# Kernel optimization log

Hardware: AMD Instinct MI355X
Metric: run time of the kernel (lower is better)

## Reference

```python
import jax, jax.numpy as jnp
import numpy as np

E, HE, HD, V, B, S, T = 512, 1024, 1024, 32000, 64, 48, 48
PAD = 0


def lstm_cell(x, h, c, Wih, Whh, b):
    # torch gate order: i, f, g, o
    g = x @ Wih.T + h @ Whh.T + b
    i, f, gg, o = jnp.split(g, 4, axis=-1)
    c2 = jax.nn.sigmoid(f) * c + jax.nn.sigmoid(i) * jnp.tanh(gg)
    h2 = jax.nn.sigmoid(o) * jnp.tanh(c2)
    return h2, c2


def run_lstm(X, mask, Wih, Whh, b):
    # X: [S,B,E], mask: [S,B] bool; emulates packed-sequence semantics:
    # carry frozen and output zeroed at padded steps.
    hsz = Whh.shape[1]
    h0 = jnp.zeros((X.shape[1], hsz), X.dtype)

    def step(carry, xm):
        h, c = carry
        x, m = xm
        h2, c2 = lstm_cell(x, h, c, Wih, Whh, b)
        m = m[:, None]
        h = jnp.where(m, h2, h)
        c = jnp.where(m, c2, c)
        return (h, c), h * m

    (hT, cT), outs = jax.lax.scan(step, (h0, h0), (X, mask))
    return outs, hT, cT


def setup_inputs() -> dict:
    key = jax.random.key(0)
    ks = jax.random.split(key, 24)

    def rn(k, shape, scale=0.05):
        return jax.random.normal(k, shape, jnp.float32) * scale

    inp = {}
    inp['source_padded'] = jax.random.randint(ks[0], (S, B), 1, V).astype(jnp.int32)
    inp['target_padded'] = jax.random.randint(ks[1], (T, B), 1, V).astype(jnp.int32)
    lens = jnp.sort(jax.random.randint(ks[2], (B,), S // 2, S + 1))[::-1]
    inp['source_lengths'] = lens.at[0].set(S).astype(jnp.int32)
    # embeddings (padding row zeroed, matching nn.Embedding padding_idx)
    inp['src_emb'] = rn(ks[3], (V, E)).at[PAD].set(0.0)
    inp['tgt_emb'] = rn(ks[4], (V, E)).at[PAD].set(0.0)
    # bidirectional encoder LSTM (b = b_ih + b_hh combined)
    inp['enc_Wih_f'] = rn(ks[5], (4 * HE, E))
    inp['enc_Whh_f'] = rn(ks[6], (4 * HE, HE))
    inp['enc_b_f'] = rn(ks[7], (4 * HE,))
    inp['enc_Wih_b'] = rn(ks[8], (4 * HE, E))
    inp['enc_Whh_b'] = rn(ks[9], (4 * HE, HE))
    inp['enc_b_b'] = rn(ks[10], (4 * HE,))
    # decoder LSTMCell
    inp['dec_Wih'] = rn(ks[11], (4 * HD, E + HD))
    inp['dec_Whh'] = rn(ks[12], (4 * HD, HD))
    inp['dec_b'] = rn(ks[13], (4 * HD,))
    # projections (all bias=False in the original)
    inp['W_h'] = rn(ks[14], (HD, 2 * HE))
    inp['W_c'] = rn(ks[15], (HD, 2 * HE))
    inp['W_att'] = rn(ks[16], (HD, 2 * HE))
    inp['W_comb'] = rn(ks[17], (HE, 2 * HE + HD))
    inp['W_vocab'] = rn(ks[18], (V, HD))
    return inp


def reference(source_padded, target_padded, source_lengths, src_emb, tgt_emb,
              enc_Wih_f, enc_Whh_f, enc_b_f, enc_Wih_b, enc_Whh_b, enc_b_b,
              dec_Wih, dec_Whh, dec_b, W_h, W_c, W_att, W_comb, W_vocab):
    # ---- encode ----
    X = src_emb[source_padded]                       # [S,B,E]
    tpos = jnp.arange(S)[:, None]
    valid = tpos < source_lengths[None, :]           # [S,B]
    fwd_out, h_f, c_f = run_lstm(X, valid, enc_Wih_f, enc_Whh_f, enc_b_f)
    # reverse each sequence within its true length (packed-seq backward dir)
    rev_idx = jnp.where(valid, source_lengths[None, :] - 1 - tpos, tpos)
    Xrev = jnp.take_along_axis(X, rev_idx[:, :, None], axis=0)
    bwd_rev, h_b, c_b = run_lstm(Xrev, valid, enc_Wih_b, enc_Whh_b, enc_b_b)
    bwd_out = jnp.take_along_axis(bwd_rev, rev_idx[:, :, None], axis=0)
    enc_hiddens = jnp.concatenate([fwd_out, bwd_out], -1).transpose(1, 0, 2)  # [B,S,2HE]
    dec_h0 = jnp.concatenate([h_f, h_b], -1) @ W_h.T  # [B,HD]
    dec_c0 = jnp.concatenate([c_f, c_b], -1) @ W_c.T
    # ---- decode ----
    enc_proj = enc_hiddens @ W_att.T                 # [B,S,HD]
    pad_mask = ~valid.T                              # [B,S], True at padding
    Y = tgt_emb[target_padded[:-1]]                  # [T-1,B,E]

    def dstep(o_prev, y):
        ybar = jnp.concatenate([y, o_prev], -1)
        # NOTE: faithful to source bug - step() is always called with
        # dec_init_state, so the LSTMCell state resets every timestep.
        h_t, c_t = lstm_cell(ybar, dec_h0, dec_c0, dec_Wih, dec_Whh, dec_b)
        e = jnp.einsum('bsh,bh->bs', enc_proj, h_t)  # multiplicative attention
        e = jnp.where(pad_mask, -jnp.inf, e)
        alpha = jax.nn.softmax(e, -1)
        a = jnp.einsum('bs,bsd->bd', alpha, enc_hiddens)   # [B,2HE]
        O = jnp.tanh(jnp.concatenate([a, h_t], -1) @ W_comb.T)  # dropout=identity (eval)
        return O, O

    o0 = jnp.zeros((B, HD), X.dtype)
    _, combined = jax.lax.scan(dstep, o0, Y)          # [T-1,B,HE]
    # ---- loss-style scores ----
    P = jax.nn.log_softmax(combined @ W_vocab.T, -1)  # [T-1,B,V]
    gold = jnp.take_along_axis(P, target_padded[1:][:, :, None], axis=-1)[..., 0]
    tmask = (target_padded[1:] != PAD).astype(P.dtype)
    return (gold * tmask).sum(0)                      # [B]
```

## Files before the change

### kernel.cpp

```cpp
#include <hip/hip_runtime.h>
#include <math.h>


#define S_    48
#define B_    64
#define E_    512
#define H_    1024
#define H4_   4096
#define V_    32000
#define T1_   47
#define NROW_ 3008
#define NROWP 3072
#define NTV_  500
#define NBE   128
#define NBD   128

typedef __bf16 bf16x8 __attribute__((ext_vector_type(8)));
typedef float  f32x4  __attribute__((ext_vector_type(4)));
typedef unsigned short ushort_t;
typedef unsigned long long ull_t;

__device__ __forceinline__ float sigm(float x){ return 1.f/(1.f+expf(-x)); }
__device__ __forceinline__ unsigned short f2bs(float f){
  unsigned u=__float_as_uint(f); u+=0x7fffu+((u>>16)&1u); return (unsigned short)(u>>16);
}
__device__ __forceinline__ float b2f(ushort_t u){ return __uint_as_float(((unsigned)u)<<16); }
__device__ __forceinline__ void gload16(const ushort_t* g, ushort_t* l){
  __builtin_amdgcn_global_load_lds((const __attribute__((address_space(1))) void*)g,
                                   (__attribute__((address_space(3))) void*)l,16,0,0);
}

__device__ __forceinline__ void ast32(void* p, unsigned v){
  __hip_atomic_store((unsigned*)p,v,__ATOMIC_RELAXED,__HIP_MEMORY_SCOPE_AGENT);
}
__device__ __forceinline__ void ast64(void* p, ull_t v){
  __hip_atomic_store((ull_t*)p,v,__ATOMIC_RELAXED,__HIP_MEMORY_SCOPE_AGENT);
}

__device__ __forceinline__ void arrive(unsigned* flags, int idx, unsigned ep){
  if(threadIdx.x==0) ast32(&flags[idx*16], ep);
}
__device__ __forceinline__ void wait_flags(unsigned* flags, int n, unsigned ep){
  for(int i=threadIdx.x;i<n;i+=256){
    while(__hip_atomic_load(&flags[i*16],__ATOMIC_RELAXED,__HIP_MEMORY_SCOPE_AGENT)<ep){}
  }
  __syncthreads();
}

__device__ __forceinline__ void stage128(const ushort_t* src, int ld, int k0,
                                         ushort_t* lds, int w, int lane){
  const int rA=lane>>3, gA=lane&7;
#pragma unroll
  for(int i=0;i<4;i++){
    int rb=w*32+i*8;
    int row=rb+rA;
    gload16(src+(size_t)row*ld+k0+(((gA)^(row&7))*8), &lds[rb*64]);
  }
}

#define ACC_DECL \
  f32x4 c00={0,0,0,0},c01={0,0,0,0},c02={0,0,0,0},c03={0,0,0,0}, \
        c10={0,0,0,0},c11={0,0,0,0},c12={0,0,0,0},c13={0,0,0,0}, \
        c20={0,0,0,0},c21={0,0,0,0},c22={0,0,0,0},c23={0,0,0,0}, \
        c30={0,0,0,0},c31={0,0,0,0},c32={0,0,0,0},c33={0,0,0,0};

#define MFMA_ __builtin_amdgcn_mfma_f32_16x16x32_bf16
#define MMA_K64(AsB,BsB) do{ \
  _Pragma("unroll") \
  for(int ks_=0;ks_<2;ks_++){ \
    const int sw_=((ks_*4+l4)^l7)*8; \
    bf16x8 a0_=*(const bf16x8*)&(AsB)[(wm*64+ 0+l15)*64+sw_]; \
    bf16x8 a1_=*(const bf16x8*)&(AsB)[(wm*64+16+l15)*64+sw_]; \
    bf16x8 a2_=*(const bf16x8*)&(AsB)[(wm*64+32+l15)*64+sw_]; \
    bf16x8 a3_=*(const bf16x8*)&(AsB)[(wm*64+48+l15)*64+sw_]; \
    bf16x8 b0_=*(const bf16x8*)&(BsB)[(wn*64+ 0+l15)*64+sw_]; \
    bf16x8 b1_=*(const bf16x8*)&(BsB)[(wn*64+16+l15)*64+sw_]; \
    bf16x8 b2_=*(const bf16x8*)&(BsB)[(wn*64+32+l15)*64+sw_]; \
    bf16x8 b3_=*(const bf16x8*)&(BsB)[(wn*64+48+l15)*64+sw_]; \
    c00=MFMA_(a0_,b0_,c00,0,0,0); c01=MFMA_(a0_,b1_,c01,0,0,0); \
    c02=MFMA_(a0_,b2_,c02,0,0,0); c03=MFMA_(a0_,b3_,c03,0,0,0); \
    c10=MFMA_(a1_,b0_,c10,0,0,0); c11=MFMA_(a1_,b1_,c11,0,0,0); \
    c12=MFMA_(a1_,b2_,c12,0,0,0); c13=MFMA_(a1_,b3_,c13,0,0,0); \
    c20=MFMA_(a2_,b0_,c20,0,0,0); c21=MFMA_(a2_,b1_,c21,0,0,0); \
    c22=MFMA_(a2_,b2_,c22,0,0,0); c23=MFMA_(a2_,b3_,c23,0,0,0); \
    c30=MFMA_(a3_,b0_,c30,0,0,0); c31=MFMA_(a3_,b1_,c31,0,0,0); \
    c32=MFMA_(a3_,b2_,c32,0,0,0); c33=MFMA_(a3_,b3_,c33,0,0,0); \
  } \
}while(0)

__global__ __launch_bounds__(256)
void proj3(const ushort_t* __restrict__ Xb, const ushort_t* __restrict__ WfB, const float* __restrict__ bf,
           const ushort_t* __restrict__ XrB, const ushort_t* __restrict__ WbB, const float* __restrict__ bb,
           const ushort_t* __restrict__ Yb, const ushort_t* __restrict__ WyB,
           float* __restrict__ XpF, float* __restrict__ XpB, float* __restrict__ Yp)
{
  __shared__ __align__(16) ushort_t As[128*64];
  __shared__ __align__(16) ushort_t Bs[128*64];
  const ushort_t* A; const ushort_t* B; const float* bias; float* C;
  if(blockIdx.z==0){A=Xb;B=WfB;bias=bf;C=XpF;}
  else if(blockIdx.z==1){A=XrB;B=WbB;bias=bb;C=XpB;}
  else {A=Yb;B=WyB;bias=nullptr;C=Yp;}
  const int tid=threadIdx.x, w=tid>>6, lane=tid&63;
  const int wm=w>>1, wn=w&1;
  const int l15=lane&15, l4=lane>>4, l7=lane&7;
  const int m0=blockIdx.x*128, n0=blockIdx.y*128;
  ACC_DECL
  for(int k0=0;k0<E_;k0+=64){
    stage128(A+(size_t)m0*E_, E_, k0, As, w, lane);
    stage128(B+(size_t)n0*E_, E_, k0, Bs, w, lane);
    __syncthreads();
    MMA_K64(As,Bs);
    __syncthreads();
  }
  const int cr=l4*4, cc=l15;
#define PSTORE(CM,mi,ni) { int col=n0+wn*64+(ni)*16+cc; float bv=bias?bias[col]:0.f; \
  _Pragma("unroll") for(int j=0;j<4;j++){ int row=m0+wm*64+(mi)*16+cr+j; \
    C[(size_t)row*H4_+col]=CM[j]+bv; } }
  PSTORE(c00,0,0) PSTORE(c01,0,1) PSTORE(c02,0,2) PSTORE(c03,0,3)
  PSTORE(c10,1,0) PSTORE(c11,1,1) PSTORE(c12,1,2) PSTORE(c13,1,3)
  PSTORE(c20,2,0) PSTORE(c21,2,1) PSTORE(c22,2,2) PSTORE(c23,2,3)
  PSTORE(c30,3,0) PSTORE(c31,3,1) PSTORE(c32,3,2) PSTORE(c33,3,3)
#undef PSTORE
}

__global__ __launch_bounds__(256)
void bproj(const ushort_t* __restrict__ A, int lda,
           const ushort_t* __restrict__ B, int ldb, int K,
           ushort_t* __restrict__ Cb)
{
  __shared__ __align__(16) ushort_t As[128*64];
  __shared__ __align__(16) ushort_t Bs[128*64];
  const int tid=threadIdx.x, w=tid>>6, lane=tid&63;
  const int wm=w>>1, wn=w&1;
  const int l15=lane&15, l4=lane>>4, l7=lane&7;
  const int m0=blockIdx.x*128, n0=blockIdx.y*128;
  ACC_DECL
  for(int k0=0;k0<K;k0+=64){
    stage128(A+(size_t)m0*lda, lda, k0, As, w, lane);
    stage128(B+(size_t)n0*ldb, ldb, k0, Bs, w, lane);
    __syncthreads();
    MMA_K64(As,Bs);
    __syncthreads();
  }
  const int cr=l4*4, cc=l15;
#define BSTORE(CM,mi,ni) { int col=n0+wn*64+(ni)*16+cc; \
  _Pragma("unroll") for(int j=0;j<4;j++){ int row=m0+wm*64+(mi)*16+cr+j; \
    Cb[(size_t)row*H_+col]=f2bs(CM[j]); } }
  BSTORE(c00,0,0) BSTORE(c01,0,1) BSTORE(c02,0,2) BSTORE(c03,0,3)
  BSTORE(c10,1,0) BSTORE(c11,1,1) BSTORE(c12,1,2) BSTORE(c13,1,3)
  BSTORE(c20,2,0) BSTORE(c21,2,1) BSTORE(c22,2,2) BSTORE(c23,2,3)
  BSTORE(c30,3,0) BSTORE(c31,3,1) BSTORE(c32,3,2) BSTORE(c33,3,3)
#undef BSTORE
}

__global__ __launch_bounds__(256)
void mfma_vocab(const ushort_t* __restrict__ A, const ushort_t* __restrict__ B,
                const int* __restrict__ tgt,
                float* __restrict__ pmax, float* __restrict__ psum, float* __restrict__ gold)
{
  __shared__ __align__(16) ushort_t As[128*64];
  __shared__ __align__(16) ushort_t Bs[128*64];
  const int tid=threadIdx.x, w=tid>>6, lane=tid&63;
  const int wm=w>>1, wn=w&1;
  const int l15=lane&15, l4=lane>>4, l7=lane&7;
  const int m0=blockIdx.x*128, n0=blockIdx.y*128;
  ACC_DECL
  for(int k0=0;k0<H_;k0+=64){
    stage128(A+(size_t)m0*H_, H_, k0, As, w, lane);
    stage128(B+(size_t)n0*H_, H_, k0, Bs, w, lane);
    __syncthreads();
    MMA_K64(As,Bs);
    __syncthreads();
  }
  const int tile=blockIdx.y*2+wn;
  const int cc=l15;
#define VEPI(mi,R0,R1,R2,R3) { \
  _Pragma("unroll") for(int j=0;j<4;j++){ \
    int row=m0+wm*64+(mi)*16+l4*4+j; \
    float m=fmaxf(fmaxf(R0[j],R1[j]),fmaxf(R2[j],R3[j])); \
    for(int o=1;o<16;o<<=1) m=fmaxf(m,__shfl_xor(m,o,64)); \
    float s=expf(R0[j]-m)+expf(R1[j]-m)+expf(R2[j]-m)+expf(R3[j]-m); \
    for(int o=1;o<16;o<<=1) s+=__shfl_xor(s,o,64); \
    if(row<NROW_){ \
      if(cc==0){ pmax[(size_t)tile*NROWP+row]=m; psum[(size_t)tile*NROWP+row]=s; } \
      int g=tgt[((row>>6)+1)*B_+(row&63)]; \
      int lj=g-(n0+wn*64); \
      if(lj>=0&&lj<64&&(lj&15)==cc){ int q=lj>>4; \
        gold[row]= (q==0)?R0[j]:(q==1)?R1[j]:(q==2)?R2[j]:R3[j]; } \
    } } }
  VEPI(0,c00,c01,c02,c03)
  VEPI(1,c10,c11,c12,c13)
  VEPI(2,c20,c21,c22,c23)
  VEPI(3,c30,c31,c32,c33)
#undef VEPI
}

__global__ __launch_bounds__(256)
void enc_persist(const ushort_t* __restrict__ WhhB2,
                 const float* __restrict__ XpF, const float* __restrict__ XpB,
                 const int* __restrict__ lens,
                 ushort_t* __restrict__ hroll,
                 float* __restrict__ cst,
                 ushort_t* __restrict__ outF, ushort_t* __restrict__ outBR,
                 unsigned* __restrict__ flagsE)
{
  __shared__ __align__(16) ushort_t Bp[64*1024];
  const int tid=threadIdx.x, w=tid>>6, lane=tid&63;
  const int blk=blockIdx.x, dir=blk>>6, j0=(blk&63)*16;
  const int l15=lane&15, l4=lane>>4;
  const ushort_t* Wd=WhhB2+(size_t)dir*H4_*H_;
  const float* xp = dir? XpB : XpF;
  float* cD = cst + (size_t)dir*65536;
  ushort_t* outD = dir? outBR : outF;
  unsigned* fD = flagsE + dir*64*16;

  for(int p=0;p<32;p++){
    int s=p*256+w*64+lane;
    int row=s>>7, g=s&127;
    int grow=((row>>4)<<10)+j0+(row&15);
    gload16(Wd+(size_t)grow*H_+((g^(row&7))*8), &Bp[(p*256+w*64)*8]);
  }
  __syncthreads();

  float hkeep[4]={0.f,0.f,0.f,0.f};

  for(int t=0;t<S_;t++){
    const ushort_t* hbR = hroll + ((size_t)t*2+dir)*65536;
    ushort_t*       hbW = hroll + ((size_t)(t+1)*2+dir)*65536;
    bf16x8 a[32];
    {
      const ushort_t* ap=hbR+(size_t)(w*16+l15)*H_+l4*8;
#pragma unroll
      for(int kk=0;kk<32;kk++) a[kk]=*(const bf16x8*)(ap+kk*32);
    }
    f32x4 acc[4];
#pragma unroll
    for(int n=0;n<4;n++) acc[n]=(f32x4){0.f,0.f,0.f,0.f};
#pragma unroll
    for(int kk=0;kk<32;kk++){
#pragma unroll
      for(int n=0;n<4;n++){
        int rb=n*16+l15;
        bf16x8 b=*(const bf16x8*)&Bp[rb*H_+(((kk*4+l4)^(rb&7))*8)];
        acc[n]=__builtin_amdgcn_mfma_f32_16x16x32_bf16(a[kk],b,acc[n],0,0,0);
      }
    }
    const int col=j0+l15;
#pragma unroll
    for(int j=0;j<4;j++){
      int row=w*16+l4*4+j;
      const float* xr=xp+(size_t)(t*64+row)*H4_;
      float g0=acc[0][j]+xr[col];
      float g1=acc[1][j]+xr[1024+col];
      float g2=acc[2][j]+xr[2048+col];
      float g3=acc[3][j]+xr[3072+col];
      size_t ix=(size_t)row*H_+col;
      float c_old=cD[ix];
      float cn=sigm(g1)*c_old+sigm(g0)*tanhf(g2);
      float hv=sigm(g3)*tanhf(cn);
      bool m=t<lens[row];
      cD[ix]= m? cn : c_old;
      hkeep[j]= m? hv : hkeep[j];
      outD[(size_t)(t*64+row)*H_+col]= m? f2bs(hv) : (ushort_t)0;
      ushort_t h16=f2bs(hkeep[j]);
      ushort_t other=(ushort_t)__shfl_xor((int)h16,1,64);
      if((lane&1)==0)
        ast32((void*)(hbW+ix), (unsigned)h16 | ((unsigned)other<<16));
    }
    __syncthreads();
    arrive(fD, blk&63, (unsigned)(t+1));
    wait_flags(fD, 64, (unsigned)(t+1));
  }
}

__global__ __launch_bounds__(256)
void dec_persist(const ushort_t* __restrict__ WoB,
                 const float* __restrict__ Yp, const float* __restrict__ whhC,
                 const float* __restrict__ dc0,
                 const ushort_t* __restrict__ encPb,
                 const ushort_t* __restrict__ Gb,
                 const ushort_t* __restrict__ WcombB,
                 const int* __restrict__ lens,
                 ushort_t* __restrict__ opRoll,
                 ushort_t* __restrict__ hRoll,
                 ushort_t* __restrict__ aGRoll,
                 ushort_t* __restrict__ combB,
                 unsigned* __restrict__ fA,
                 unsigned* __restrict__ fB,
                 unsigned* __restrict__ fC)
{
  __shared__ __align__(16) ushort_t Bp[32*1024];
  __shared__ __align__(16) ushort_t WcHp[16*1024];
  __shared__ float gbuf[64*32];
  __shared__ float es[S_], al[S_];
  const int tid=threadIdx.x, w=tid>>6, lane=tid&63;
  const int blk=blockIdx.x;
  const int l15=lane&15, l4=lane>>4;
  const int j0=blk*8;
  const int b=blk;
  const int j0c=(blk-64)*16;

  for(int p=0;p<16;p++){
    int s=p*256+w*64+lane;
    int row=s>>7, g=s&127;
    int grow=((row>>3)<<10)+j0+(row&7);
    gload16(WoB+(size_t)grow*H_+((g^(row&7))*8), &Bp[(p*256+w*64)*8]);
  }
  if(blk>=64){
    for(int p=0;p<8;p++){
      int s=p*256+w*64+lane;
      int row=s>>7, g=s&127;
      gload16(WcombB+(size_t)(j0c+row)*3072+2048+((g^(row&7))*8), &WcHp[(p*256+w*64)*8]);
    }
  }
  __syncthreads();

  f32x4 accP=(f32x4){0.f,0.f,0.f,0.f};
  for(int t=0;t<T1_;t++){
    const unsigned ept=(unsigned)(t+1);
    const ushort_t* opT = opRoll + (size_t)t*65536;
    ushort_t*       opW = opRoll + (size_t)(t+1)*65536;
    ushort_t*       hT  = hRoll  + (size_t)t*65536;
    ushort_t*       aGT = aGRoll + (size_t)t*65536;
    {
      bf16x8 a[32];
      {
        const ushort_t* ap=opT+(size_t)(w*16+l15)*H_+l4*8;
#pragma unroll
        for(int kk=0;kk<32;kk++) a[kk]=*(const bf16x8*)(ap+kk*32);
      }
      f32x4 acc0=(f32x4){0.f,0.f,0.f,0.f}, acc1=(f32x4){0.f,0.f,0.f,0.f};
#pragma unroll
      for(int kk=0;kk<32;kk++){
        int rb0=l15, rb1=16+l15;
        bf16x8 b0=*(const bf16x8*)&Bp[rb0*1024+(((kk*4+l4)^(rb0&7))*8)];
        bf16x8 b1=*(const bf16x8*)&Bp[rb1*1024+(((kk*4+l4)^(rb1&7))*8)];
        acc0=__builtin_amdgcn_mfma_f32_16x16x32_bf16(a[kk],b0,acc0,0,0,0);
        acc1=__builtin_amdgcn_mfma_f32_16x16x32_bf16(a[kk],b1,acc1,0,0,0);
      }
#pragma unroll
      for(int j=0;j<4;j++){
        gbuf[(w*16+l4*4+j)*32 + l15   ]=acc0[j];
        gbuf[(w*16+l4*4+j)*32 + 16+l15]=acc1[j];
      }
      __syncthreads();
      {
        int o=tid*2, row=o>>3, c=o&7;
        float hv2[2];
#pragma unroll
        for(int q=0;q<2;q++){
          int cc=c+q;
          float g0=gbuf[row*32+cc], g1=gbuf[row*32+8+cc],
                g2=gbuf[row*32+16+cc], g3=gbuf[row*32+24+cc];
          const float* yr=Yp+(size_t)(t*64+row)*H4_;
          const float* wr=whhC+(size_t)row*H4_;
          g0+=yr[j0+cc]     +wr[j0+cc];
          g1+=yr[1024+j0+cc]+wr[1024+j0+cc];
          g2+=yr[2048+j0+cc]+wr[2048+j0+cc];
          g3+=yr[3072+j0+cc]+wr[3072+j0+cc];
          float cn=sigm(g1)*dc0[(size_t)row*H_+j0+cc]+sigm(g0)*tanhf(g2);
          hv2[q]=sigm(g3)*tanhf(cn);
        }
        unsigned pk=(unsigned)f2bs(hv2[0]) | ((unsigned)f2bs(hv2[1])<<16);
        ast32((void*)(hT+(size_t)row*H_+j0+c), pk);
      }
    }
    __syncthreads();
    arrive(fA, blk, ept);
    wait_flags(fA, 128, ept);

    if(blk<64){
      float hreg[16];
      {
        const ushort_t* hp=hT+(size_t)b*H_+lane*16;
        bf16x8 h0=*(const bf16x8*)hp, h1=*(const bf16x8*)(hp+8);
#pragma unroll
        for(int i=0;i<8;i++){ hreg[i]=b2f(((const ushort_t*)&h0)[i]);
                              hreg[8+i]=b2f(((const ushort_t*)&h1)[i]); }
      }
      for(int s=w;s<S_;s+=4){
        const ushort_t* epr=encPb+((size_t)b*S_+s)*H_+lane*16;
        bf16x8 e0=*(const bf16x8*)epr, e1=*(const bf16x8*)(epr+8);
        float sum=0.f;
#pragma unroll
        for(int i=0;i<8;i++) sum+=b2f(((const ushort_t*)&e0)[i])*hreg[i]
                                +b2f(((const ushort_t*)&e1)[i])*hreg[8+i];
        for(int o=32;o>0;o>>=1) sum+=__shfl_xor(sum,o,64);
        if(lane==0) es[s]=sum;
      }
      __syncthreads();
      if(tid<64){
        int L=lens[b];
        float e=(tid<S_&&tid<L)? es[tid] : -INFINITY;
        float m=e;
        for(int o=32;o>0;o>>=1) m=fmaxf(m,__shfl_xor(m,o,64));
        float p=(tid<S_)? expf(e-m):0.f;
        float sm=p;
        for(int o=32;o>0;o>>=1) sm+=__shfl_xor(sm,o,64);
        if(tid<S_) al[tid]=p/sm;
      }
      __syncthreads();
      {
        float r0=0.f,r1=0.f,r2=0.f,r3=0.f;
        const int c4=tid*4;
        for(int s=0;s<S_;s++){
          float aa=al[s];
          ushort4 g4=*(const ushort4*)(Gb+((size_t)b*S_+s)*H_+c4);
          r0+=aa*b2f(g4.x); r1+=aa*b2f(g4.y); r2+=aa*b2f(g4.z); r3+=aa*b2f(g4.w);
        }
        ull_t pk=(ull_t)f2bs(r0) | ((ull_t)f2bs(r1)<<16)
               | ((ull_t)f2bs(r2)<<32) | ((ull_t)f2bs(r3)<<48);
        ast64((void*)(aGT+(size_t)b*H_+c4), pk);
      }
      __syncthreads();
      arrive(fB, blk, ept);
      wait_flags(fC, 64, ept);
    } else {
      bf16x8 a[32];
      {
        const ushort_t* ap=hT+(size_t)(w*16+l15)*H_+l4*8;
#pragma unroll
        for(int kk=0;kk<32;kk++) a[kk]=*(const bf16x8*)(ap+kk*32);
      }
      accP=(f32x4){0.f,0.f,0.f,0.f};
#pragma unroll
      for(int kk=0;kk<32;kk++){
        bf16x8 bb=*(const bf16x8*)&WcHp[l15*1024+(((kk*4+l4)^(l15&7))*8)];
        accP=__builtin_amdgcn_mfma_f32_16x16x32_bf16(a[kk],bb,accP,0,0,0);
      }
      wait_flags(fB, 64, ept);
#pragma unroll
      for(int j=0;j<4;j++){
        int row=w*16+l4*4+j, col=j0c+l15;
        float av=b2f(aGT[(size_t)row*H_+col]);
        float o=tanhf(accP[j]+av);
        ushort_t ob=f2bs(o);
        combB[((size_t)t*64+row)*H_+col]=ob;
        ushort_t other=(ushort_t)__shfl_xor((int)ob,1,64);
        if((lane&1)==0)
          ast32((void*)(opW+(size_t)row*H_+col), (unsigned)ob | ((unsigned)other<<16));
      }
      __syncthreads();
      arrive(fC, blk-64, ept);
      wait_flags(fC, 64, ept);
    }
  }
}

__global__ void embed_all(const int* __restrict__ src, const int* __restrict__ tgt,
                          const int* __restrict__ lens,
                          const float* __restrict__ se, const float* __restrict__ te,
                          ushort_t* __restrict__ X, ushort_t* __restrict__ Xr,
                          ushort_t* __restrict__ Y)
{
  int bi=blockIdx.x, tid=threadIdx.x;
  const float* srcrow; ushort_t* dst;
  if(bi<3072){
    int s=bi>>6, b=bi&63;
    srcrow=se+(size_t)src[s*64+b]*E_; dst=X+(size_t)bi*E_;
  } else if(bi<6144){
    int r=bi-3072, t=r>>6, b=r&63;
    int L=lens[b]; int ts=(t<L)? L-1-t : t;
    srcrow=se+(size_t)src[ts*64+b]*E_; dst=Xr+(size_t)r*E_;
  } else {
    int r=bi-6144, t=r>>6, b=r&63;
    srcrow=te+(size_t)tgt[t*64+b]*E_; dst=Y+(size_t)r*E_;
  }
  float4 v=((const float4*)srcrow)[tid];
  ushort4 o; o.x=f2bs(v.x); o.y=f2bs(v.y); o.z=f2bs(v.z); o.w=f2bs(v.w);
  ((ushort4*)dst)[tid]=o;
}

__global__ void prep_w(const float* __restrict__ Whhf,const float* __restrict__ Whhb,
                       const float* __restrict__ Wihf,const float* __restrict__ Wihb,
                       const float* __restrict__ Watt,const float* __restrict__ dWih,
                       const float* __restrict__ Wcomb,
                       ushort_t* __restrict__ WhhfB,ushort_t* __restrict__ WhhbB,
                       ushort_t* __restrict__ WihfB,ushort_t* __restrict__ WihbB,
                       ushort_t* __restrict__ WattB,ushort_t* __restrict__ dWihYb,
                       ushort_t* __restrict__ dWihOb,ushort_t* __restrict__ WcombB)
{
  const int NQ=6029312;
  for(int q=blockIdx.x*256+threadIdx.x; q<NQ; q+=gridDim.x*256){
    const float* src; ushort_t* dst; size_t si,di; int r;
    if(q<1048576){ si=(size_t)q*4; src=Whhf; dst=WhhfB; di=si; }
    else if(q<2097152){ r=q-1048576; si=(size_t)r*4; src=Whhb; dst=WhhbB; di=si; }
    else if(q<2621440){ r=q-2097152; si=(size_t)r*4; src=Wihf; dst=WihfB; di=si; }
    else if(q<3145728){ r=q-2621440; si=(size_t)r*4; src=Wihb; dst=WihbB; di=si; }
    else if(q<3670016){ r=q-3145728; si=(size_t)r*4; src=Watt; dst=WattB; di=si; }
    else if(q<4194304){ r=q-3670016; int row=r>>7, c4=(r&127)*4;
                        si=(size_t)row*1536+c4; src=dWih; dst=dWihYb; di=(size_t)row*512+c4; }
    else if(q<5242880){ r=q-4194304; int row=r>>8, c4=(r&255)*4;
                        si=(size_t)row*1536+512+c4; src=dWih; dst=dWihOb; di=(size_t)row*1024+c4; }
    else { r=q-5242880; si=(size_t)r*4; src=Wcomb; dst=WcombB; di=si; }
    float4 v=*(const float4*)(src+si);
    ushort4 o; o.x=f2bs(v.x);o.y=f2bs(v.y);o.z=f2bs(v.z);o.w=f2bs(v.w);
    *(ushort4*)(dst+di)=o;
  }
}

__global__ void f2b_voc(const float* __restrict__ in, ushort_t* __restrict__ out){
  for(size_t q=blockIdx.x*256+threadIdx.x; q<8192000; q+=(size_t)gridDim.x*256){
    float4 v=*(const float4*)(in+q*4);
    ushort4 o; o.x=f2bs(v.x);o.y=f2bs(v.y);o.z=f2bs(v.z);o.w=f2bs(v.w);
    *(ushort4*)(out+q*4)=o;
  }
}

__global__ void gather_concat(const ushort_t* __restrict__ outF, const ushort_t* __restrict__ outBR,
                              const int* __restrict__ lens,
                              const ushort_t* __restrict__ hb, const float* __restrict__ cst,
                              ushort_t* __restrict__ encHb,
                              float* __restrict__ hcat, float* __restrict__ ccat)
{
  int bi=blockIdx.x, tid=threadIdx.x;
  if(bi<3072){
    int b=bi/48, s=bi%48;
    int L=lens[b]; int sr=(s<L)? L-1-s : s;
    ((ushort4*)(encHb+(size_t)bi*2048))[tid]      =((const ushort4*)(outF +(size_t)(s*64+b)*H_))[tid];
    ((ushort4*)(encHb+(size_t)bi*2048+1024))[tid] =((const ushort4*)(outBR+(size_t)(sr*64+b)*H_))[tid];
  } else {
    int b=bi-3072;
    for(int i=tid;i<H_;i+=256){
      hcat[(size_t)b*2048+i]      = b2f(hb[(size_t)b*H_+i]);
      hcat[(size_t)b*2048+1024+i] = b2f(hb[65536+(size_t)b*H_+i]);
      ccat[(size_t)b*2048+i]      = cst[(size_t)b*H_+i];
      ccat[(size_t)b*2048+1024+i] = cst[65536+(size_t)b*H_+i];
    }
  }
}

template<int BM,int BN,int TM,int TN>
__global__ __launch_bounds__(256)
void gemm_nt(int M, int K,
             const float* __restrict__ A, int lda,
             const float* __restrict__ B, int ldb,
             float* __restrict__ C, int ldc,
             const float* __restrict__ bias)
{
  constexpr int BK=16;
  __shared__ float As[BK][BM+4];
  __shared__ float Bs[BK][BN+4];
  const int tid=threadIdx.x;
  constexpr int TX=BN/TN;
  const int tx=tid%TX, ty=tid/TX;
  const int m0=blockIdx.x*BM, n0=blockIdx.y*BN;
  float acc[TM][TN];
#pragma unroll
  for(int i=0;i<TM;i++)
#pragma unroll
    for(int j=0;j<TN;j++) acc[i][j]=0.f;
  for(int k0=0;k0<K;k0+=BK){
    for(int i=tid;i<BM*4;i+=256){
      int r=i>>2, c=(i&3)*4;
      float4 v=make_float4(0.f,0.f,0.f,0.f);
      if(m0+r<M) v=*(const float4*)(A+(size_t)(m0+r)*lda+k0+c);
      As[c+0][r]=v.x; As[c+1][r]=v.y; As[c+2][r]=v.z; As[c+3][r]=v.w;
    }
    for(int i=tid;i<BN*4;i+=256){
      int r=i>>2, c=(i&3)*4;
      float4 v=*(const float4*)(B+(size_t)(n0+r)*ldb+k0+c);
      Bs[c+0][r]=v.x; Bs[c+1][r]=v.y; Bs[c+2][r]=v.z; Bs[c+3][r]=v.w;
    }
    __syncthreads();
#pragma unroll
    for(int k=0;k<BK;k++){
      float a[TM], bb[TN];
#pragma unroll
      for(int i=0;i<TM;i++) a[i]=As[k][ty*TM+i];
#pragma unroll
      for(int j=0;j<TN;j++) bb[j]=Bs[k][tx*TN+j];
#pragma unroll
      for(int i=0;i<TM;i++)
#pragma unroll
        for(int j=0;j<TN;j++) acc[i][j]+=a[i]*bb[j];
    }
    __syncthreads();
  }
#pragma unroll
  for(int i=0;i<TM;i++){
    int r=m0+ty*TM+i;
    if(r>=M) continue;
#pragma unroll
    for(int j=0;j<TN;j++){
      int c=n0+tx*TN+j;
      float v=acc[i][j];
      if(bias) v+=bias[c];
      C[(size_t)r*ldc+c]=v;
    }
  }
}

__global__ __launch_bounds__(256)
void lse_final(const float* __restrict__ pmax, const float* __restrict__ psum,
               const float* __restrict__ gold, float* __restrict__ gl)
{
  int r=blockIdx.x*256+threadIdx.x;
  if(r>=NROW_) return;
  float M=-INFINITY, S=0.f;
  for(int i=0;i<NTV_;i++){
    float m2=pmax[(size_t)i*NROWP+r];
    float s2=psum[(size_t)i*NROWP+r];
    float Mn=fmaxf(M,m2);
    S = S*expf(M-Mn) + s2*expf(m2-Mn);
    M=Mn;
  }
  gl[r]=gold[r]-(M+logf(S));
}

__global__ void final_sum(const float* __restrict__ gl, const int* __restrict__ tgt,
                          float* __restrict__ out)
{
  int b=threadIdx.x;
  float acc=0.f;
  for(int t=0;t<T1_;t++){
    int tk=tgt[(t+1)*B_+b];
    if(tk!=0) acc+=gl[t*B_+b];
  }
  out[b]=acc;
}

extern "C" void kernel_launch(void* const* d_in, const int* in_sizes, int n_in,
                              void* d_out, int out_size, void* d_ws, size_t ws_size,
                              hipStream_t stream)
{
  (void)in_sizes; (void)n_in; (void)out_size; (void)ws_size;
  const int*   src    =(const int*)  d_in[0];
  const int*   tgt    =(const int*)  d_in[1];
  const int*   lens   =(const int*)  d_in[2];
  const float* src_emb=(const float*)d_in[3];
  const float* tgt_emb=(const float*)d_in[4];
  const float* Wih_f  =(const float*)d_in[5];
  const float* Whh_f  =(const float*)d_in[6];
  const float* b_f    =(const float*)d_in[7];
  const float* Wih_b  =(const float*)d_in[8];
  const float* Whh_b  =(const float*)d_in[9];
  const float* b_b    =(const float*)d_in[10];
  const float* dWih   =(const float*)d_in[11];
  const float* dWhh   =(const float*)d_in[12];
  const float* db     =(const float*)d_in[13];
  const float* W_h    =(const float*)d_in[14];
  const float* W_c    =(const float*)d_in[15];
  const float* W_att  =(const float*)d_in[16];
  const float* W_comb =(const float*)d_in[17];
  const float* W_voc  =(const float*)d_in[18];
  float* out=(float*)d_out;
  float* W  =(float*)d_ws;

  size_t off=0;
  auto AL=[&](size_t n){ size_t o=off; off+=n; return o; };
  const size_t oXpF  =AL((size_t)3072*H4_);
  const size_t oXpB  =AL((size_t)3072*H4_);
  const size_t oYp   =AL((size_t)3072*H4_);
  const size_t oCst  =AL((size_t)2*64*H_);
  const size_t oHcat =AL((size_t)64*2048);
  const size_t oCcat =AL((size_t)64*2048);
  const size_t oDh0  =AL((size_t)64*H_);
  const size_t oDc0  =AL((size_t)64*H_);
  const size_t oWhhC =AL((size_t)64*H4_);
  const size_t oBar  =AL((size_t)8192);
  const size_t oXb    =AL((size_t)3072*E_/2);
  const size_t oXrb   =AL((size_t)3072*E_/2);
  const size_t oYb    =AL((size_t)3072*E_/2);
  const size_t oWhhfB =AL((size_t)H4_*H_/2);
  const size_t oWhhbB =AL((size_t)H4_*H_/2);
  const size_t oWihfB =AL((size_t)H4_*E_/2);
  const size_t oWihbB =AL((size_t)H4_*E_/2);
  const size_t oWattB =AL((size_t)H_*2048/2);
  const size_t odWihYb=AL((size_t)H4_*E_/2);
  const size_t odWihOb=AL((size_t)H4_*H_/2);
  const size_t oWcombB=AL((size_t)H_*3072/2);
  const size_t oOutF  =AL((size_t)S_*64*H_/2);
  const size_t oOutBR =AL((size_t)S_*64*H_/2);
  const size_t oEncHb =AL((size_t)3072*2048/2);
  const size_t oEncPb =AL((size_t)3072*H_/2);

  ushort_t* Xb    =(ushort_t*)(W+oXb);
  ushort_t* Xrb   =(ushort_t*)(W+oXrb);
  ushort_t* Yb    =(ushort_t*)(W+oYb);
  ushort_t* WhhfB =(ushort_t*)(W+oWhhfB);
  ushort_t* WihfB =(ushort_t*)(W+oWihfB);
  ushort_t* WihbB =(ushort_t*)(W+oWihbB);
  ushort_t* WattB =(ushort_t*)(W+oWattB);
  ushort_t* dWihYb=(ushort_t*)(W+odWihYb);
  ushort_t* dWihOb=(ushort_t*)(W+odWihOb);
  ushort_t* WcombB=(ushort_t*)(W+oWcombB);
  ushort_t* OutF  =(ushort_t*)(W+oOutF);
  ushort_t* OutBR =(ushort_t*)(W+oOutBR);
  ushort_t* EncHb =(ushort_t*)(W+oEncHb);
  ushort_t* EncPb =(ushort_t*)(W+oEncPb);
  ushort_t* WvocB =(ushort_t*)(W+oXpF);
  float* pmax = W+oXpF+16450000;
  float* psum = pmax + (size_t)NTV_*NROWP;
  ushort_t* Gbuf  =(ushort_t*)(W+oXpF+19550000);
  ushort_t* OpRoll=(ushort_t*)(W+oXpF+21150000);
  ushort_t* HRoll =(ushort_t*)(W+oXpF+22750000);
  float* gold = W+oXpF+24400000;
  float* gl   = gold + NROWP;
  ushort_t* AGRoll=OutBR;
  ushort_t* HrollE=EncHb;
  ushort_t* HbFin =HrollE+(size_t)S_*2*65536;
  ushort_t* CombB =(ushort_t*)(W+oOutF);
  unsigned* flagsE=(unsigned*)(W+oBar);
  unsigned* fA = flagsE + 2*64*16;
  unsigned* fB = fA + 128*16;
  unsigned* fC = fB + 64*16;

  hipMemsetAsync(W+oBar, 0, 8192*sizeof(float), stream);
  hipMemsetAsync(W+oCst, 0, (size_t)2*64*H_*sizeof(float), stream);
  hipMemsetAsync(HrollE, 0, (size_t)2*65536*sizeof(ushort_t), stream);

  embed_all<<<dim3(3072+3072+NROW_),128,0,stream>>>(src,tgt,lens,src_emb,tgt_emb,Xb,Xrb,Yb);
  prep_w<<<dim3(2048),256,0,stream>>>(Whh_f,Whh_b,Wih_f,Wih_b,W_att,dWih,W_comb,
                                      WhhfB,(ushort_t*)(W+oWhhbB),WihfB,WihbB,WattB,
                                      dWihYb,dWihOb,WcombB);
  proj3<<<dim3(24,32,3),256,0,stream>>>(Xb,WihfB,b_f, Xrb,WihbB,b_b, Yb,dWihYb,
                                        W+oXpF,W+oXpB,W+oYp);

  enc_persist<<<dim3(NBE),256,0,stream>>>(WhhfB, W+oXpF, W+oXpB, lens,
                                          HrollE, W+oCst, OutF, OutBR, flagsE);

  hipMemsetAsync(OpRoll, 0, (size_t)65536*sizeof(ushort_t), stream);

  gather_concat<<<dim3(3136),256,0,stream>>>(OutF,OutBR,lens,HbFin,W+oCst,
                                             EncHb,W+oHcat,W+oCcat);
  f2b_voc<<<dim3(2048),256,0,stream>>>(W_voc, WvocB);
  bproj<<<dim3(24,8),256,0,stream>>>(EncHb,2048, WattB,2048, 2048, EncPb);
  bproj<<<dim3(24,8),256,0,stream>>>(EncHb,2048, WcombB,3072, 2048, Gbuf);
  gemm_nt<64,64,4,4><<<dim3(1,16),256,0,stream>>>(64,2048, W+oHcat,2048, W_h,2048, W+oDh0,H_, nullptr);
  gemm_nt<64,64,4,4><<<dim3(1,16),256,0,stream>>>(64,2048, W+oCcat,2048, W_c,2048, W+oDc0,H_, nullptr);
  gemm_nt<64,64,4,4><<<dim3(1,64),256,0,stream>>>(64,H_, W+oDh0,H_, dWhh,H_, W+oWhhC,H4_, db);

  dec_persist<<<dim3(NBD),256,0,stream>>>(dWihOb, W+oYp, W+oWhhC, W+oDc0,
                                          EncPb, Gbuf, WcombB, lens,
                                          OpRoll, HRoll, AGRoll, CombB, fA, fB, fC);

  mfma_vocab<<<dim3(24,250),256,0,stream>>>(CombB, WvocB, tgt, pmax, psum, gold);
  lse_final<<<dim3((NROW_+255)/256),256,0,stream>>>(pmax, psum, gold, gl);
  final_sum<<<dim3(1),64,0,stream>>>(gl, tgt, out);
}
```

Before: 2.604 ms.

## Store input projections in bf16, cache decoder constants in LDS, sleep in spin-wait

The proj3 outputs (encoder and decoder input-gate projections) are now written as bf16 instead of fp32, which halves the bytes the persistent encoder and decoder kernels read each step. The decoder persistent kernel preloads its slice of the constant whhC and dc0 into shared memory once, so the per-step gate math no longer rereads them from global memory. The flag spin-wait now issues s_sleep between polls to reduce memory contention. The trade-offs are bf16 rounding on the gate pre-activations and possibly slightly longer wake-up latency at barriers.

```diff
diff --git a/kernel.cpp b/kernel.cpp
--- a/kernel.cpp
+++ b/kernel.cpp
@@ -42,7 +42,8 @@
 }
 __device__ __forceinline__ void wait_flags(unsigned* flags, int n, unsigned ep){
   for(int i=threadIdx.x;i<n;i+=256){
-    while(__hip_atomic_load(&flags[i*16],__ATOMIC_RELAXED,__HIP_MEMORY_SCOPE_AGENT)<ep){}
+    while(__hip_atomic_load(&flags[i*16],__ATOMIC_RELAXED,__HIP_MEMORY_SCOPE_AGENT)<ep)
+      __builtin_amdgcn_s_sleep(1);
   }
   __syncthreads();
 }
@@ -92,11 +93,11 @@
 void proj3(const ushort_t* __restrict__ Xb, const ushort_t* __restrict__ WfB, const float* __restrict__ bf,
            const ushort_t* __restrict__ XrB, const ushort_t* __restrict__ WbB, const float* __restrict__ bb,
            const ushort_t* __restrict__ Yb, const ushort_t* __restrict__ WyB,
-           float* __restrict__ XpF, float* __restrict__ XpB, float* __restrict__ Yp)
+           ushort_t* __restrict__ XpF, ushort_t* __restrict__ XpB, ushort_t* __restrict__ Yp)
 {
   __shared__ __align__(16) ushort_t As[128*64];
   __shared__ __align__(16) ushort_t Bs[128*64];
-  const ushort_t* A; const ushort_t* B; const float* bias; float* C;
+  const ushort_t* A; const ushort_t* B; const float* bias; ushort_t* C;
   if(blockIdx.z==0){A=Xb;B=WfB;bias=bf;C=XpF;}
   else if(blockIdx.z==1){A=XrB;B=WbB;bias=bb;C=XpB;}
   else {A=Yb;B=WyB;bias=nullptr;C=Yp;}
@@ -115,7 +116,7 @@
   const int cr=l4*4, cc=l15;
 #define PSTORE(CM,mi,ni) { int col=n0+wn*64+(ni)*16+cc; float bv=bias?bias[col]:0.f; \
   _Pragma("unroll") for(int j=0;j<4;j++){ int row=m0+wm*64+(mi)*16+cr+j; \
-    C[(size_t)row*H4_+col]=CM[j]+bv; } }
+    C[(size_t)row*H4_+col]=f2bs(CM[j]+bv); } }
   PSTORE(c00,0,0) PSTORE(c01,0,1) PSTORE(c02,0,2) PSTORE(c03,0,3)
   PSTORE(c10,1,0) PSTORE(c11,1,1) PSTORE(c12,1,2) PSTORE(c13,1,3)
   PSTORE(c20,2,0) PSTORE(c21,2,1) PSTORE(c22,2,2) PSTORE(c23,2,3)
@@ -197,7 +198,7 @@
 
 __global__ __launch_bounds__(256)
 void enc_persist(const ushort_t* __restrict__ WhhB2,
-                 const float* __restrict__ XpF, const float* __restrict__ XpB,
+                 const ushort_t* __restrict__ XpF, const ushort_t* __restrict__ XpB,
                  const int* __restrict__ lens,
                  ushort_t* __restrict__ hroll,
                  float* __restrict__ cst,
@@ -209,7 +210,7 @@
   const int blk=blockIdx.x, dir=blk>>6, j0=(blk&63)*16;
   const int l15=lane&15, l4=lane>>4;
   const ushort_t* Wd=WhhB2+(size_t)dir*H4_*H_;
-  const float* xp = dir? XpB : XpF;
+  const ushort_t* xp = dir? XpB : XpF;
   float* cD = cst + (size_t)dir*65536;
   ushort_t* outD = dir? outBR : outF;
   unsigned* fD = flagsE + dir*64*16;
@@ -249,11 +250,11 @@
 #pragma unroll
     for(int j=0;j<4;j++){
       int row=w*16+l4*4+j;
-      const float* xr=xp+(size_t)(t*64+row)*H4_;
-      float g0=acc[0][j]+xr[col];
-      float g1=acc[1][j]+xr[1024+col];
-      float g2=acc[2][j]+xr[2048+col];
-      float g3=acc[3][j]+xr[3072+col];
+      const ushort_t* xr=xp+(size_t)(t*64+row)*H4_;
+      float g0=acc[0][j]+b2f(xr[col]);
+      float g1=acc[1][j]+b2f(xr[1024+col]);
+      float g2=acc[2][j]+b2f(xr[2048+col]);
+      float g3=acc[3][j]+b2f(xr[3072+col]);
       size_t ix=(size_t)row*H_+col;
       float c_old=cD[ix];
       float cn=sigm(g1)*c_old+sigm(g0)*tanhf(g2);
@@ -275,7 +276,8 @@
 
 __global__ __launch_bounds__(256)
 void dec_persist(const ushort_t* __restrict__ WoB,
-                 const float* __restrict__ Yp, const float* __restrict__ whhC,
+                 const ushort_t* __restrict__ Yp,
+                 const float* __restrict__ whhC,
                  const float* __restrict__ dc0,
                  const ushort_t* __restrict__ encPb,
                  const ushort_t* __restrict__ Gb,
@@ -292,6 +294,8 @@
   __shared__ __align__(16) ushort_t Bp[32*1024];
   __shared__ __align__(16) ushort_t WcHp[16*1024];
   __shared__ float gbuf[64*32];
+  __shared__ float whhCs[64*32];
+  __shared__ float dc0s[64*8];
   __shared__ float es[S_], al[S_];
   const int tid=threadIdx.x, w=tid>>6, lane=tid&63;
   const int blk=blockIdx.x;
@@ -313,6 +317,12 @@
       gload16(WcombB+(size_t)(j0c+row)*3072+2048+((g^(row&7))*8), &WcHp[(p*256+w*64)*8]);
     }
   }
+  for(int p=0;p<8;p++){
+    int s=p*256+tid;
+    int row=s>>5, gc=s&31, gate=gc>>3, c=gc&7;
+    whhCs[s]=whhC[(size_t)row*H4_+gate*1024+j0+c];
+  }
+  if(tid<512){ int row=tid>>3, c=tid&7; dc0s[tid]=dc0[(size_t)row*H_+j0+c]; }
   __syncthreads();
 
   f32x4 accP=(f32x4){0.f,0.f,0.f,0.f};
@@ -346,19 +356,16 @@
       __syncthreads();
       {
         int o=tid*2, row=o>>3, c=o&7;
+        const ushort_t* ypr=Yp+(size_t)(t*64+row)*H4_;
         float hv2[2];
 #pragma unroll
         for(int q=0;q<2;q++){
           int cc=c+q;
-          float g0=gbuf[row*32+cc], g1=gbuf[row*32+8+cc],
-                g2=gbuf[row*32+16+cc], g3=gbuf[row*32+24+cc];
-          const float* yr=Yp+(size_t)(t*64+row)*H4_;
-          const float* wr=whhC+(size_t)row*H4_;
-          g0+=yr[j0+cc]     +wr[j0+cc];
-          g1+=yr[1024+j0+cc]+wr[1024+j0+cc];
-          g2+=yr[2048+j0+cc]+wr[2048+j0+cc];
-          g3+=yr[3072+j0+cc]+wr[3072+j0+cc];
-          float cn=sigm(g1)*dc0[(size_t)row*H_+j0+cc]+sigm(g0)*tanhf(g2);
+          float g0=gbuf[row*32+cc]   +b2f(ypr[j0+cc])     +whhCs[row*32+cc];
+          float g1=gbuf[row*32+8+cc] +b2f(ypr[1024+j0+cc])+whhCs[row*32+8+cc];
+          float g2=gbuf[row*32+16+cc]+b2f(ypr[2048+j0+cc])+whhCs[row*32+16+cc];
+          float g3=gbuf[row*32+24+cc]+b2f(ypr[3072+j0+cc])+whhCs[row*32+24+cc];
+          float cn=sigm(g1)*dc0s[row*8+cc]+sigm(g0)*tanhf(g2);
           hv2[q]=sigm(g3)*tanhf(cn);
         }
         unsigned pk=(unsigned)f2bs(hv2[0]) | ((unsigned)f2bs(hv2[1])<<16);
@@ -689,6 +696,9 @@
   ushort_t* OutBR =(ushort_t*)(W+oOutBR);
   ushort_t* EncHb =(ushort_t*)(W+oEncHb);
   ushort_t* EncPb =(ushort_t*)(W+oEncPb);
+  ushort_t* XpFb  =(ushort_t*)(W+oXpF);
+  ushort_t* XpBb  =(ushort_t*)(W+oXpB);
+  ushort_t* YpB   =(ushort_t*)(W+oYp);
   ushort_t* WvocB =(ushort_t*)(W+oXpF);
   float* pmax = W+oXpF+16450000;
   float* psum = pmax + (size_t)NTV_*NROWP;
@@ -715,9 +725,9 @@
                                       WhhfB,(ushort_t*)(W+oWhhbB),WihfB,WihbB,WattB,
                                       dWihYb,dWihOb,WcombB);
   proj3<<<dim3(24,32,3),256,0,stream>>>(Xb,WihfB,b_f, Xrb,WihbB,b_b, Yb,dWihYb,
-                                        W+oXpF,W+oXpB,W+oYp);
-
-  enc_persist<<<dim3(NBE),256,0,stream>>>(WhhfB, W+oXpF, W+oXpB, lens,
+                                        XpFb,XpBb,YpB);
+
+  enc_persist<<<dim3(NBE),256,0,stream>>>(WhhfB, XpFb, XpBb, lens,
                                           HrollE, W+oCst, OutF, OutBR, flagsE);
 
   hipMemsetAsync(OpRoll, 0, (size_t)65536*sizeof(ushort_t), stream);
@@ -731,7 +741,7 @@
   gemm_nt<64,64,4,4><<<dim3(1,16),256,0,stream>>>(64,2048, W+oCcat,2048, W_c,2048, W+oDc0,H_, nullptr);
   gemm_nt<64,64,4,4><<<dim3(1,64),256,0,stream>>>(64,H_, W+oDh0,H_, dWhh,H_, W+oWhhC,H4_, db);
 
-  dec_persist<<<dim3(NBD),256,0,stream>>>(dWihOb, W+oYp, W+oWhhC, W+oDc0,
+  dec_persist<<<dim3(NBD),256,0,stream>>>(dWihOb, YpB, W+oWhhC, W+oDc0,
                                           EncPb, Gbuf, WcombB, lens,
                                           OpRoll, HRoll, AGRoll, CombB, fA, fB, fC);
 
```

Measured after the change: 2.612 ms. About the same (+0.3%).
